# Optimization experiments

Measured on AMD Instinct MI355X. Metric: run time of the kernel, lower is better.

Reference implementation:

```python
import jax, jax.numpy as jnp
import numpy as np

BSZ, N, D = 32, 243, 544   # batch, frames, embed dim (17 joints * 32)
H = 8                      # heads
HD = D // H                # head dim = 68
NS = 17                    # number of seeds (joints)
UP = 2                     # ExAttention up_ratio
MLP1 = 4 * D               # Block MLP hidden (mlp_ratio=4)
MLP2 = 2 * D               # ExtBaseBlock MLP hidden (mlp_ratio=2)


def _ln(x, g, b):
    m = x.mean(-1, keepdims=True)
    v = ((x - m) ** 2).mean(-1, keepdims=True)
    return (x - m) * jax.lax.rsqrt(v + 1e-5) * g + b


def _lin(x, W, b=None):
    y = x @ W.T
    return y if b is None else y + b


def _mlp(x, w1, b1, w2, b2):
    return _lin(jax.nn.gelu(_lin(x, w1, b1), approximate=False), w2, b2)


def setup_inputs() -> dict:
    key = jax.random.key(0)
    ks = jax.random.split(key, 40)
    i = iter(range(40))
    r = lambda shape, s=0.02: jax.random.normal(ks[next(i)], shape, jnp.float32) * s
    inp = {
        'x': jax.random.normal(ks[next(i)], (BSZ, N, D), jnp.float32),
        'seed': jax.random.normal(ks[next(i)], (NS, D), jnp.float32),
        # --- RelativeAttention block (use_swin=True, qkv_bias=False) ---
        'ln1_g': jnp.ones((D,), jnp.float32), 'ln1_b': jnp.zeros((D,), jnp.float32),
        'w_qkv': r((3 * D, D)),
        'w_proj': r((D, D)), 'b_proj': jnp.zeros((D,), jnp.float32),
        'b_table': r((1, H, 2 * N - 1)),  # trunc_normal std=0.02 table
        'ln2_g': jnp.ones((D,), jnp.float32), 'ln2_b': jnp.zeros((D,), jnp.float32),
        'mlp_w1': r((MLP1, D)), 'mlp_b1': jnp.zeros((MLP1,), jnp.float32),
        'mlp_w2': r((D, MLP1)), 'mlp_b2': jnp.zeros((D,), jnp.float32),
        # --- ExtBaseBlock (ExAttention, up_ratio=2, mlp_ratio=2) ---
        'eln1_g': jnp.ones((D,), jnp.float32), 'eln1_b': jnp.zeros((D,), jnp.float32),
        'w_trans': r((UP * D, D)), 'b_trans': jnp.zeros((UP * D,), jnp.float32),
        'w0': r((UP * D, D)), 'b0': jnp.zeros((UP * D,), jnp.float32),
        'w1': r((UP * D, D)), 'b1': jnp.zeros((UP * D,), jnp.float32),
        'w_proj2': r((D, UP * D)), 'b_proj2': jnp.zeros((D,), jnp.float32),
        'eln2_g': jnp.ones((D,), jnp.float32), 'eln2_b': jnp.zeros((D,), jnp.float32),
        'emlp_w1': r((MLP2, D)), 'emlp_b1': jnp.zeros((MLP2,), jnp.float32),
        'emlp_w2': r((D, MLP2)), 'emlp_b2': jnp.zeros((D,), jnp.float32),
    }
    return inp


def reference(x, seed, ln1_g, ln1_b, w_qkv, w_proj, b_proj, b_table,
              ln2_g, ln2_b, mlp_w1, mlp_b1, mlp_w2, mlp_b2,
              eln1_g, eln1_b, w_trans, b_trans, w0, b0, w1, b1,
              w_proj2, b_proj2, eln2_g, eln2_b, emlp_w1, emlp_b1, emlp_w2, emlp_b2):
    Bsz, Nn, C = x.shape
    # ---------- Block with RelativeAttention (use_swin=True) ----------
    h = _ln(x, ln1_g, ln1_b)
    qkv = _lin(h, w_qkv).reshape(Bsz, Nn, 3, H, HD).transpose(2, 0, 3, 1, 4)
    q, k, v = qkv[0], qkv[1], qkv[2]                        # (B,H,N,hd)
    # Swin-style relative position bias gather: B_index[i,j] = i - j + N - 1
    idx = jnp.arange(Nn)[:, None] - jnp.arange(Nn)[None, :] + (Nn - 1)
    bias = b_table[:, :, idx]                               # (1,H,N,N)
    attn = jax.nn.softmax(jnp.einsum('bhid,bhjd->bhij', q, k) * (HD ** -0.5) + bias, axis=-1)
    o = jnp.einsum('bhij,bhjd->bhid', attn, v).transpose(0, 2, 1, 3).reshape(Bsz, Nn, C)
    x = x + _lin(o, w_proj, b_proj)
    x = x + _mlp(_ln(x, ln2_g, ln2_b), mlp_w1, mlp_b1, mlp_w2, mlp_b2)
    # ---------- ExtBaseBlock with ExAttention (double-softmax external memory) ----------
    h = _ln(x, eln1_g, eln1_b)
    uc = UP * C // H                                         # per-head up dim = 136
    xu = _lin(h, w_trans, b_trans).reshape(Bsz, Nn, H, uc).transpose(0, 2, 1, 3)  # (B,H,F,uc)
    s0 = _lin(seed, w0, b0).reshape(NS, H, uc).transpose(1, 0, 2)                 # (H,NS,uc)
    a = jnp.einsum('bhfc,hnc->bhfn', xu, s0)                 # (B,H,F,NS)
    a = jax.nn.softmax(a, axis=-2)                           # softmax over frame axis
    a = a / (1e-7 + a.sum(-1, keepdims=True))                # renormalize over seeds
    mean_attn = a.mean(axis=(0, 1, 2))                       # (NS,)
    s1 = _lin(seed, w1, b1).reshape(NS, H, uc).transpose(1, 0, 2)                 # (H,NS,uc)
    o = jnp.einsum('bhfn,hnc->bhfc', a, s1).transpose(0, 2, 1, 3).reshape(Bsz, Nn, UP * C)
    x = x + _lin(o, w_proj2, b_proj2)
    x = x + _mlp(_ln(x, eln2_g, eln2_b), emlp_w1, emlp_b1, emlp_w2, emlp_b2)
    return x, mean_attn
```

## Files before the change

### kernel.cpp

```cpp
#include <hip/hip_runtime.h>
#include <math.h>
#include <stdint.h>

#define BSZd 32
#define NTOK 243
#define DIMd 544
#define NH 8
#define HDd 68
#define NSEED 17
#define UPDd 1088
#define UCd 136
#define MROWS (BSZd*NTOK)
#define BND ((size_t)MROWS*DIMd)
#define QPP 24576
#define KPOFF ((size_t)256*QPP)
#define VTP 20480
#define PBP 65536
#define BUFE (128*32)
#define SLICE 6144

typedef __bf16 bfx8 __attribute__((ext_vector_type(8)));
typedef __bf16 bfx4 __attribute__((ext_vector_type(4)));
typedef float  fx4  __attribute__((ext_vector_type(4)));

#define GLOAD_LDS(g, l) __builtin_amdgcn_global_load_lds( \
    (__attribute__((address_space(1))) void*)(g), \
    (__attribute__((address_space(3))) void*)(l), 16, 0, 0)

__device__ __forceinline__ void mfma_core(const __bf16* __restrict__ A, int lda,
        const __bf16* __restrict__ W, int ldb, int K,
        __bf16* __restrict__ As, __bf16* __restrict__ Bs, fx4 acc[4][4]) {
    const int tid = threadIdx.x;
    const int lane = tid & 63, wave = tid >> 6;
    const int r = lane >> 2, cp = lane & 3;
    const int c = cp ^ (r & 3) ^ ((r >> 2) & 1);
    const __bf16* Ag0 = A + (size_t)(wave * 32 + r) * lda + c * 8;
    const __bf16* Ag1 = Ag0 + (size_t)16 * lda;
    const __bf16* Wg0 = W + (size_t)(wave * 32 + r) * ldb + c * 8;
    const __bf16* Wg1 = Wg0 + (size_t)16 * ldb;
    const int wr0 = (wave * 32) * 32;
    const int wr1 = (wave * 32 + 16) * 32;
    const int fl = lane & 15, q = lane >> 4;
    const int wm = (wave & 1) * 64, wn = (wave >> 1) * 64;
    const int sw = (fl & 3) ^ ((fl >> 2) & 1);
    const int IT = K >> 5;
    GLOAD_LDS(Ag0, As + wr0);
    GLOAD_LDS(Ag1, As + wr1);
    GLOAD_LDS(Wg0, Bs + wr0);
    GLOAD_LDS(Wg1, Bs + wr1);
    for (int kit = 0; kit < IT; kit++) {
        const int p = kit & 1;
        __syncthreads();
        if (kit + 1 < IT) {
            const int np = 1 - p;
            const int off = (kit + 1) * 32;
            GLOAD_LDS(Ag0 + off, As + np * BUFE + wr0);
            GLOAD_LDS(Ag1 + off, As + np * BUFE + wr1);
            GLOAD_LDS(Wg0 + off, Bs + np * BUFE + wr0);
            GLOAD_LDS(Wg1 + off, Bs + np * BUFE + wr1);
        }
        const __bf16* Ab = As + p * BUFE;
        const __bf16* Bb = Bs + p * BUFE;
        bfx8 af[4], bfr[4];
        #pragma unroll
        for (int i = 0; i < 4; i++) {
            int m = wm + i * 16 + fl;
            af[i] = *(const bfx8*)(Ab + (m * 4 + (q ^ sw)) * 8);
            int n = wn + i * 16 + fl;
            bfr[i] = *(const bfx8*)(Bb + (n * 4 + (q ^ sw)) * 8);
        }
        #pragma unroll
        for (int i = 0; i < 4; i++)
            #pragma unroll
            for (int j = 0; j < 4; j++)
                acc[i][j] = __builtin_amdgcn_mfma_f32_16x16x32_bf16(af[i], bfr[j], acc[i][j], 0, 0, 0);
    }
}

struct Cvt8 {
    const float* src[8];
    __bf16* dst[8];
    int nreal[8];
    int rows[8];
    int K[8];
};
__global__ __launch_bounds__(256) void cvt_all(Cvt8 d) {
    int blk = blockIdx.x;
    int seg = 0, base = 0;
    while (seg < 7 && blk - base >= d.rows[seg]) { base += d.rows[seg]; seg++; }
    int n = blk - base;
    int K = d.K[seg];
    __bf16* drow = d.dst[seg] + (size_t)n * K;
    if (n < d.nreal[seg]) {
        const float* srow = d.src[seg] + (size_t)n * K;
        for (int k = threadIdx.x * 4; k < K; k += 1024) {
            float4 v = *(const float4*)(srow + k);
            bfx4 o; o[0]=(__bf16)v.x; o[1]=(__bf16)v.y; o[2]=(__bf16)v.z; o[3]=(__bf16)v.w;
            *(bfx4*)(drow + k) = o;
        }
    } else {
        bfx4 z = {(__bf16)0.f,(__bf16)0.f,(__bf16)0.f,(__bf16)0.f};
        for (int k = threadIdx.x * 4; k < K; k += 1024) *(bfx4*)(drow + k) = z;
    }
}

__global__ __launch_bounds__(256) void zero4(float4* __restrict__ p, int n4) {
    float4 z = make_float4(0.f, 0.f, 0.f, 0.f);
    for (int i = blockIdx.x * 256 + threadIdx.x; i < n4; i += gridDim.x * 256)
        p[i] = z;
}

__global__ __launch_bounds__(256) void ln_kernel(const float* __restrict__ x,
        const float* __restrict__ g, const float* __restrict__ bb, __bf16* __restrict__ out) {
    int row = blockIdx.x;
    const float* xr = x + (size_t)row * DIMd;
    __bf16* orow = out + (size_t)row * DIMd;
    int tid = threadIdx.x;
    float e0 = xr[tid];
    float e1 = xr[tid + 256];
    float e2 = (tid < DIMd - 512) ? xr[tid + 512] : 0.f;
    float s  = e0 + e1 + e2;
    float sq = e0*e0 + e1*e1 + e2*e2;
    __shared__ float sa[4], sb[4];
    for (int off = 32; off; off >>= 1) { s += __shfl_down(s, off, 64); sq += __shfl_down(sq, off, 64); }
    int lane = tid & 63, w = tid >> 6;
    if (lane == 0) { sa[w] = s; sb[w] = sq; }
    __syncthreads();
    if (tid == 0) { sa[0] = sa[0]+sa[1]+sa[2]+sa[3]; sb[0] = sb[0]+sb[1]+sb[2]+sb[3]; }
    __syncthreads();
    s = sa[0]; sq = sb[0];
    float mean = s * (1.f / DIMd);
    float var  = sq * (1.f / DIMd) - mean * mean;
    float rstd = rsqrtf(var + 1e-5f);
    orow[tid]       = (__bf16)((e0 - mean) * rstd * g[tid]       + bb[tid]);
    orow[tid + 256] = (__bf16)((e1 - mean) * rstd * g[tid + 256] + bb[tid + 256]);
    if (tid < DIMd - 512)
        orow[tid + 512] = (__bf16)((e2 - mean) * rstd * g[tid + 512] + bb[tid + 512]);
}

template<int ACT, int HAS_BIAS, int HAS_RES, int OUTMODE>
__global__ __launch_bounds__(256) void mgemm(
        const __bf16* __restrict__ A, int lda, const __bf16* __restrict__ W, int ldb,
        const float* __restrict__ bias, const float* __restrict__ res,
        void* __restrict__ Cv, int M, int Mtiles, int Nreal, int K, int Cstride,
        __bf16* __restrict__ qQK, __bf16* __restrict__ qVt) {
    const int L = blockIdx.y * gridDim.x + blockIdx.x;
    const int xcd = L & 7, s = L >> 3;
    const int kk2 = s / gridDim.x, j2 = s - kk2 * gridDim.x;
    const int mt = kk2 * 8 + xcd;
    if (mt >= Mtiles) return;
    const int m0 = mt * 64, n0 = j2 * 128;
    __shared__ __bf16 Smem[2 * SLICE];
    const int tid = threadIdx.x, lane = tid & 63, w = tid >> 6;
    const __bf16* Gs[3];
    int dbase[3];
    #pragma unroll
    for (int it = 0; it < 3; it++) {
        int ch = w * 192 + it * 64 + lane;
        int row = ch >> 2, cp2 = ch & 3;
        int cc = cp2 ^ (row & 3) ^ ((row >> 2) & 1);
        dbase[it] = (w * 192 + it * 64) * 8;
        Gs[it] = (row < 64) ? A + (size_t)(m0 + row) * lda + cc * 8
                            : W + (size_t)(n0 + row - 64) * ldb + cc * 8;
    }
    const int fl = lane & 15, q = lane >> 4;
    const int wm = (w & 1) * 32, wn = (w >> 1) * 64;
    const int sw = (fl & 3) ^ ((fl >> 2) & 1);
    const int IT = K >> 5;
    fx4 acc[2][4];
    #pragma unroll
    for (int i = 0; i < 2; i++)
        #pragma unroll
        for (int j = 0; j < 4; j++)
            acc[i][j] = (fx4){0.f, 0.f, 0.f, 0.f};
    #pragma unroll
    for (int it = 0; it < 3; it++)
        GLOAD_LDS(Gs[it], Smem + dbase[it]);
    for (int kit = 0; kit < IT; kit++) {
        const int p = kit & 1;
        __syncthreads();
        if (kit + 1 < IT) {
            const int np = 1 - p;
            const int koff = (kit + 1) * 32;
            #pragma unroll
            for (int it = 0; it < 3; it++)
                GLOAD_LDS(Gs[it] + koff, Smem + np * SLICE + dbase[it]);
        }
        const __bf16* Ab = Smem + p * SLICE;
        const __bf16* Bb = Ab + 2048;
        bfx8 af[2], bfr[4];
        #pragma unroll
        for (int i = 0; i < 2; i++) {
            int m = wm + i * 16 + fl;
            af[i] = *(const bfx8*)(Ab + (m * 4 + (q ^ sw)) * 8);
        }
        #pragma unroll
        for (int j = 0; j < 4; j++) {
            int n = wn + j * 16 + fl;
            bfr[j] = *(const bfx8*)(Bb + (n * 4 + (q ^ sw)) * 8);
        }
        #pragma unroll
        for (int i = 0; i < 2; i++)
            #pragma unroll
            for (int j = 0; j < 4; j++)
                acc[i][j] = __builtin_amdgcn_mfma_f32_16x16x32_bf16(af[i], bfr[j], acc[i][j], 0, 0, 0);
    }
    #pragma unroll
    for (int i = 0; i < 2; i++)
        #pragma unroll
        for (int v = 0; v < 4; v++) {
            int row = m0 + wm + i * 16 + q * 4 + v;
            if (row >= M) continue;
            #pragma unroll
            for (int j = 0; j < 4; j++) {
                int col = n0 + wn + j * 16 + fl;
                if (col >= Nreal) continue;
                float val = acc[i][j][v];
                if (HAS_BIAS) val += bias[col];
                if (ACT == 1) val = 0.5f * val * (1.f + erff(val * 0.70710678118654752f));
                if (HAS_RES)  val += res[(size_t)row * Cstride + col];
                if (OUTMODE == 2) {
                    int t = col / DIMd, rem = col - t * DIMd;
                    int hh = rem / HDd, hd = rem - hh * HDd;
                    int b = row / NTOK, tok = row - b * NTOK;
                    int bh = b * 8 + hh;
                    if (t == 0)      qQK[(size_t)bh * QPP + tok * 96 + hd] = (__bf16)val;
                    else if (t == 1) qQK[KPOFF + (size_t)bh * QPP + tok * 96 + hd] = (__bf16)val;
                    else             qVt[(size_t)bh * VTP + hd * 256 + tok] = (__bf16)val;
                } else if (OUTMODE == 1) {
                    ((__bf16*)Cv)[(size_t)row * Cstride + col] = (__bf16)val;
                } else {
                    ((float*)Cv)[(size_t)row * Cstride + col] = val;
                }
            }
        }
}

__global__ __launch_bounds__(256) void gemm32_kernel(
        const float* __restrict__ A, const float* __restrict__ W,
        const float* __restrict__ bias, float* __restrict__ C, int M, int Nn, int K) {
    __shared__ __align__(16) float As[16][68];
    __shared__ __align__(16) float Ws[16][68];
    int tid = threadIdx.x;
    int tx = tid & 15, ty = tid >> 4;
    int m0 = blockIdx.y * 64, n0 = blockIdx.x * 64;
    float acc[4][4] = {};
    int lr = tid >> 2, lk = (tid & 3) << 2;
    for (int k0 = 0; k0 < K; k0 += 16) {
        float4 av = make_float4(0.f,0.f,0.f,0.f), wv = make_float4(0.f,0.f,0.f,0.f);
        int gm = m0 + lr, gn = n0 + lr, gk = k0 + lk;
        if (gm < M)  av = *(const float4*)(A + (size_t)gm * K + gk);
        if (gn < Nn) wv = *(const float4*)(W + (size_t)gn * K + gk);
        __syncthreads();
        As[lk+0][lr]=av.x; As[lk+1][lr]=av.y; As[lk+2][lr]=av.z; As[lk+3][lr]=av.w;
        Ws[lk+0][lr]=wv.x; Ws[lk+1][lr]=wv.y; Ws[lk+2][lr]=wv.z; Ws[lk+3][lr]=wv.w;
        __syncthreads();
        #pragma unroll
        for (int kk = 0; kk < 16; kk++) {
            float4 a4 = *(const float4*)&As[kk][ty << 2];
            float4 b4 = *(const float4*)&Ws[kk][tx << 2];
            float ar[4] = {a4.x, a4.y, a4.z, a4.w};
            float br[4] = {b4.x, b4.y, b4.z, b4.w};
            #pragma unroll
            for (int i = 0; i < 4; i++)
                #pragma unroll
                for (int j = 0; j < 4; j++)
                    acc[i][j] = fmaf(ar[i], br[j], acc[i][j]);
        }
    }
    #pragma unroll
    for (int i = 0; i < 4; i++) {
        int gm = m0 + (ty << 2) + i;
        if (gm >= M) continue;
        #pragma unroll
        for (int j = 0; j < 4; j++) {
            int gn = n0 + (tx << 2) + j;
            if (gn >= Nn) continue;
            C[(size_t)gm * Nn + gn] = acc[i][j] + bias[gn];
        }
    }
}

__global__ __launch_bounds__(256) void attn_escore(const __bf16* __restrict__ Qp,
        const float* __restrict__ bt, __bf16* __restrict__ Pb, float* __restrict__ rs) {
    __shared__ __bf16 Qs[128 * 96];
    __shared__ __bf16 Ks[256 * 96];
    __shared__ float sumb[128 * 2];
    const int mh = blockIdx.x, bh = blockIdx.y, h = bh & 7;
    const int tid = threadIdx.x, lane = tid & 63, w = tid >> 6;
    const int fl = lane & 15, q = lane >> 4;
    const int wm = (w & 1) * 64, wn = (w >> 1) * 128;
    const __bf16* Qg = Qp + (size_t)bh * QPP + (size_t)mh * 128 * 96;
    const __bf16* Kg = Qp + KPOFF + (size_t)bh * QPP;
    #pragma unroll
    for (int it = 0; it < 6; it++) {
        int Lc = (w * 6 + it) * 64 + lane;
        int r = Lc / 12, sl = Lc - r * 12, c = sl ^ (r & 3);
        GLOAD_LDS(Qg + r * 96 + c * 8, Qs + Lc * 8);
    }
    #pragma unroll
    for (int it = 0; it < 12; it++) {
        int Lc = (w * 12 + it) * 64 + lane;
        int r = Lc / 12, sl = Lc - r * 12, c = sl ^ (r & 3);
        GLOAD_LDS(Kg + r * 96 + c * 8, Ks + Lc * 8);
    }
    __syncthreads();
    fx4 acc[4][8];
    #pragma unroll
    for (int i = 0; i < 4; i++)
        #pragma unroll
        for (int jj = 0; jj < 8; jj++)
            acc[i][jj] = (fx4){0.f, 0.f, 0.f, 0.f};
    #pragma unroll
    for (int kk = 0; kk < 3; kk++) {
        bfx8 af[4], bfr[8];
        #pragma unroll
        for (int i = 0; i < 4; i++) {
            int rA = wm + i * 16 + fl, cA = kk * 4 + q;
            af[i] = *(const bfx8*)(Qs + (rA * 12 + (cA ^ (rA & 3))) * 8);
        }
        #pragma unroll
        for (int jj = 0; jj < 8; jj++) {
            int rB = wn + jj * 16 + fl, cB = kk * 4 + q;
            bfr[jj] = *(const bfx8*)(Ks + (rB * 12 + (cB ^ (rB & 3))) * 8);
        }
        #pragma unroll
        for (int i = 0; i < 4; i++)
            #pragma unroll
            for (int jj = 0; jj < 8; jj++)
                acc[i][jj] = __builtin_amdgcn_mfma_f32_16x16x32_bf16(af[i], bfr[jj], acc[i][jj], 0, 0, 0);
    }
    const float scale = 0.121267812518166f;
    const float* btr = bt + h * (2 * NTOK - 1);
    __bf16* Pp = Pb + (size_t)bh * PBP + (size_t)mh * 128 * 256;
    #pragma unroll
    for (int i = 0; i < 4; i++)
        #pragma unroll
        for (int v = 0; v < 4; v++) {
            int lr = wm + i * 16 + q * 4 + v;
            int gm = mh * 128 + lr;
            float sm = 0.f;
            #pragma unroll
            for (int jj = 0; jj < 8; jj++) {
                int gn = wn + jj * 16 + fl;
                float e = 0.f;
                if (gm < NTOK && gn < NTOK)
                    e = expf(acc[i][jj][v] * scale + btr[gm - gn + NTOK - 1]);
                acc[i][jj][v] = e;
                sm += e;
                Pp[(size_t)lr * 256 + gn] = (__bf16)e;
            }
            #pragma unroll
            for (int msk = 1; msk < 16; msk <<= 1)
                sm += __shfl_xor(sm, msk, 64);
            if (fl == 0) sumb[lr * 2 + (w >> 1)] = sm;
        }
    __syncthreads();
    if (tid < 128)
        rs[(size_t)bh * 256 + mh * 128 + tid] = sumb[tid * 2] + sumb[tid * 2 + 1];
}

__global__ __launch_bounds__(256) void attn_pv2(const __bf16* __restrict__ Pb,
        const __bf16* __restrict__ Vt, const float* __restrict__ rs,
        __bf16* __restrict__ o) {
    __shared__ __bf16 As[2 * BUFE];
    __shared__ __bf16 Bs[2 * BUFE];
    const int mt = blockIdx.x, bh = blockIdx.y, b = bh >> 3, h = bh & 7;
    const int tid = threadIdx.x, lane = tid & 63, wave = tid >> 6;
    fx4 acc[4][4];
    #pragma unroll
    for (int i = 0; i < 4; i++)
        #pragma unroll
        for (int j = 0; j < 4; j++)
            acc[i][j] = (fx4){0.f, 0.f, 0.f, 0.f};
    mfma_core(Pb + (size_t)bh * PBP + (size_t)mt * 128 * 256, 256,
              Vt + (size_t)bh * VTP, 256, 256, As, Bs, acc);
    const int fl = lane & 15, q = lane >> 4;
    const int wm = (wave & 1) * 64, wn = (wave >> 1) * 64;
    #pragma unroll
    for (int i = 0; i < 4; i++)
        #pragma unroll
        for (int v = 0; v < 4; v++) {
            int gm = mt * 128 + wm + i * 16 + q * 4 + v;
            if (gm >= NTOK) continue;
            float inv = 1.f / rs[(size_t)bh * 256 + gm];
            #pragma unroll
            for (int j = 0; j < 4; j++) {
                int col = wn + j * 16 + fl;
                if (col >= HDd) continue;
                o[((size_t)(b * NTOK + gm)) * DIMd + h * HDd + col] = (__bf16)(acc[i][j][v] * inv);
            }
        }
}

__global__ __launch_bounds__(256) void scatter_s0big(const float* __restrict__ S0f,
        __bf16* __restrict__ W) {
    int hn = blockIdx.x;
    __bf16* row = W + (size_t)hn * UPDd;
    int h = hn / NSEED, n = hn - h * NSEED;
    for (int j = threadIdx.x; j < UPDd; j += 256) {
        __bf16 v = (__bf16)0.f;
        if (hn < 136 && (j / UCd) == h) v = (__bf16)S0f[(size_t)n * UPDd + j];
        row[j] = v;
    }
}

__global__ __launch_bounds__(256) void scatter_s1bigT(const float* __restrict__ S1f,
        __bf16* __restrict__ W) {
    int j = blockIdx.x;
    __bf16* row = W + (size_t)j * 160;
    int hj = j / UCd;
    int t = threadIdx.x;
    if (t < 160) {
        __bf16 v = (__bf16)0.f;
        if (j < UPDd && t < 136) {
            int h = t / NSEED, n = t - h * NSEED;
            if (h == hj) v = (__bf16)S1f[(size_t)n * UPDd + j];
        }
        row[t] = v;
    }
}

__global__ __launch_bounds__(256) void seed_softmax2(float* __restrict__ a2) {
    int col = blockIdx.x, b = blockIdx.y;
    float* base = a2 + (size_t)b * NTOK * 136 + col;
    int f = threadIdx.x;
    __shared__ float rbuf[4];
    float v = (f < NTOK) ? base[(size_t)f * 136] : -1e30f;
    float m = v;
    for (int off = 32; off; off >>= 1) m = fmaxf(m, __shfl_down(m, off, 64));
    int lane = f & 63, w = f >> 6;
    if (lane == 0) rbuf[w] = m;
    __syncthreads();
    m = fmaxf(fmaxf(rbuf[0], rbuf[1]), fmaxf(rbuf[2], rbuf[3]));
    float e = (f < NTOK) ? expf(v - m) : 0.f;
    float s = e;
    for (int off = 32; off; off >>= 1) s += __shfl_down(s, off, 64);
    __syncthreads();
    if (lane == 0) rbuf[w] = s;
    __syncthreads();
    float denom = rbuf[0] + rbuf[1] + rbuf[2] + rbuf[3];
    if (f < NTOK) base[(size_t)f * 136] = e / denom;
}

__global__ void zero_kernel(float* p, int n) {
    int i = blockIdx.x * blockDim.x + threadIdx.x;
    if (i < n) p[i] = 0.f;
}

__global__ __launch_bounds__(256) void seed_renorm(const float* __restrict__ a2,
        __bf16* __restrict__ a2b, float* __restrict__ part) {
    int f = blockIdx.x, b = blockIdx.y;
    int t = threadIdx.x;
    __shared__ float vals[136];
    __shared__ float hinv[8];
    __shared__ float nsum[NSEED];
    if (t < NSEED) nsum[t] = 0.f;
    const float* arow = a2 + ((size_t)(b * NTOK + f)) * 136;
    if (t < 136) vals[t] = arow[t];
    __syncthreads();
    if (t < 8) {
        float s = 0.f;
        #pragma unroll
        for (int n = 0; n < NSEED; n++) s += vals[t * NSEED + n];
        hinv[t] = 1.f / (1e-7f + s);
    }
    __syncthreads();
    __bf16* brow = a2b + ((size_t)(b * NTOK + f)) * 160;
    if (t < 160) {
        if (t < 136) {
            float wv = vals[t] * hinv[t / NSEED];
            brow[t] = (__bf16)wv;
            atomicAdd(&nsum[t % NSEED], wv);
        } else brow[t] = (__bf16)0.f;
    }
    __syncthreads();
    if (t < NSEED) atomicAdd(&part[b * NSEED + t], nsum[t]);
}

__global__ void mean_final(const float* __restrict__ part, float* __restrict__ mean_attn) {
    int n = threadIdx.x;
    if (n < NSEED) {
        float s = 0.f;
        for (int b = 0; b < BSZd; b++) s += part[b * NSEED + n];
        mean_attn[n] = s * (1.f / (BSZd * NH * NTOK));
    }
}

extern "C" void kernel_launch(void* const* d_in, const int* in_sizes, int n_in,
                              void* d_out, int out_size, void* d_ws, size_t ws_size,
                              hipStream_t stream) {
    (void)in_sizes; (void)n_in; (void)out_size; (void)ws_size;
    const float* x       = (const float*)d_in[0];
    const float* seed    = (const float*)d_in[1];
    const float* ln1_g   = (const float*)d_in[2];
    const float* ln1_b   = (const float*)d_in[3];
    const float* w_qkv   = (const float*)d_in[4];
    const float* w_proj  = (const float*)d_in[5];
    const float* b_proj  = (const float*)d_in[6];
    const float* b_table = (const float*)d_in[7];
    const float* ln2_g   = (const float*)d_in[8];
    const float* ln2_b   = (const float*)d_in[9];
    const float* mlp_w1  = (const float*)d_in[10];
    const float* mlp_b1  = (const float*)d_in[11];
    const float* mlp_w2  = (const float*)d_in[12];
    const float* mlp_b2  = (const float*)d_in[13];
    const float* eln1_g  = (const float*)d_in[14];
    const float* eln1_b  = (const float*)d_in[15];
    const float* w_trans = (const float*)d_in[16];
    const float* b_trans = (const float*)d_in[17];
    const float* w0      = (const float*)d_in[18];
    const float* b0      = (const float*)d_in[19];
    const float* w1      = (const float*)d_in[20];
    const float* b1      = (const float*)d_in[21];
    const float* w_proj2 = (const float*)d_in[22];
    const float* b_proj2 = (const float*)d_in[23];
    const float* eln2_g  = (const float*)d_in[24];
    const float* eln2_b  = (const float*)d_in[25];
    const float* emlp_w1 = (const float*)d_in[26];
    const float* emlp_b1 = (const float*)d_in[27];
    const float* emlp_w2 = (const float*)d_in[28];
    const float* emlp_b2 = (const float*)d_in[29];

    char* wsb = (char*)d_ws;
    __bf16* Wq  = (__bf16*)(wsb);
    __bf16* Wp  = (__bf16*)(wsb + 1810432);
    __bf16* Wm1 = (__bf16*)(wsb + 2506752);
    __bf16* Wm2 = (__bf16*)(wsb + 4874240);
    __bf16* Wt  = (__bf16*)(wsb + 7659520);
    __bf16* Wp2 = (__bf16*)(wsb + 8912896);
    __bf16* We1 = (__bf16*)(wsb + 10305536);
    __bf16* We2 = (__bf16*)(wsb + 11558912);
    __bf16* Abf = (__bf16*)(wsb + 12951552);
    float*  F1  = (float*) (wsb + 21446656);
    float*  F2  = (float*) (wsb + 38367232);
    char*   RegBig = wsb + 55287808;
    char*   RegS   = wsb + 89266176;
    __bf16* Qp  = (__bf16*)RegBig;
    __bf16* Pb  = (__bf16*)F1;
    __bf16* Vt  = (__bf16*)RegS;
    float*  rsb = (float*)(RegS + 10485760);
    __bf16* Tb   = (__bf16*)RegBig;
    __bf16* XU   = (__bf16*)RegBig;
    __bf16* O2   = (__bf16*)(RegBig + 16920576);
    __bf16* T2   = (__bf16*)RegBig;
    float*  a2    = (float*)RegS;
    __bf16* a2b   = (__bf16*)(RegS + 4230144);
    float*  S0f   = (float*)(RegS + 6728704);
    float*  S1f   = (float*)(RegS + 6802688);
    __bf16* S0big = (__bf16*)(RegS + 6876672);
    __bf16* S1bigT= (__bf16*)(RegS + 7433728);
    float*  mean_part = (float*)(RegS + 7802368);
    float* xout = (float*)d_out;
    float* mean_attn = xout + BND;

    dim3 blk(256);
    Cvt8 cd;
    cd.src[0]=w_qkv;  cd.dst[0]=Wq;  cd.nreal[0]=1632; cd.rows[0]=1664; cd.K[0]=544;
    cd.src[1]=w_proj; cd.dst[1]=Wp;  cd.nreal[1]=544;  cd.rows[1]=640;  cd.K[1]=544;
    cd.src[2]=mlp_w1; cd.dst[2]=Wm1; cd.nreal[2]=2176; cd.rows[2]=2176; cd.K[2]=544;
    cd.src[3]=mlp_w2; cd.dst[3]=Wm2; cd.nreal[3]=544;  cd.rows[3]=640;  cd.K[3]=2176;
    cd.src[4]=w_trans;cd.dst[4]=Wt;  cd.nreal[4]=1088; cd.rows[4]=1152; cd.K[4]=544;
    cd.src[5]=w_proj2;cd.dst[5]=Wp2; cd.nreal[5]=544;  cd.rows[5]=640;  cd.K[5]=1088;
    cd.src[6]=emlp_w1;cd.dst[6]=We1; cd.nreal[6]=1088; cd.rows[6]=1152; cd.K[6]=544;
    cd.src[7]=emlp_w2;cd.dst[7]=We2; cd.nreal[7]=544;  cd.rows[7]=640;  cd.K[7]=1088;
    cvt_all<<<8704, blk, 0, stream>>>(cd);
    zero4<<<1024, blk, 0, stream>>>((float4*)Qp, 1572864);
    zero4<<<1024, blk, 0, stream>>>((float4*)Vt, 655360);
    ln_kernel<<<MROWS, blk, 0, stream>>>(x, ln1_g, ln1_b, Abf);
    mgemm<0,0,0,2><<<dim3(13,128), blk, 0, stream>>>(Abf, 544, Wq, 544, nullptr, nullptr, nullptr, MROWS, 122, 1632, 544, 0, Qp, Vt);
    attn_escore<<<dim3(2,256), blk, 0, stream>>>(Qp, b_table, Pb, rsb);
    attn_pv2<<<dim3(2,256), blk, 0, stream>>>(Pb, Vt, rsb, Abf);
    mgemm<0,1,1,0><<<dim3(5,128), blk, 0, stream>>>(Abf, 544, Wp, 544, b_proj, x, F1, MROWS, 122, 544, 544, 544, nullptr, nullptr);
    ln_kernel<<<MROWS, blk, 0, stream>>>(F1, ln2_g, ln2_b, Abf);
    mgemm<1,1,0,1><<<dim3(17,128), blk, 0, stream>>>(Abf, 544, Wm1, 544, mlp_b1, nullptr, Tb, MROWS, 122, 2176, 544, 2176, nullptr, nullptr);
    mgemm<0,1,1,0><<<dim3(5,128), blk, 0, stream>>>(Tb, 2176, Wm2, 2176, mlp_b2, F1, F2, MROWS, 122, 544, 2176, 544, nullptr, nullptr);
    ln_kernel<<<MROWS, blk, 0, stream>>>(F2, eln1_g, eln1_b, Abf);
    mgemm<0,1,0,1><<<dim3(9,128), blk, 0, stream>>>(Abf, 544, Wt, 544, b_trans, nullptr, XU, MROWS, 122, 1088, 544, 1088, nullptr, nullptr);
    gemm32_kernel<<<dim3(17,1), blk, 0, stream>>>(seed, w0, b0, S0f, NSEED, UPDd, DIMd);
    gemm32_kernel<<<dim3(17,1), blk, 0, stream>>>(seed, w1, b1, S1f, NSEED, UPDd, DIMd);
    scatter_s0big<<<256, blk, 0, stream>>>(S0f, S0big);
    scatter_s1bigT<<<1152, blk, 0, stream>>>(S1f, S1bigT);
    mgemm<0,0,0,0><<<dim3(2,128), blk, 0, stream>>>(XU, 1088, S0big, 1088, nullptr, nullptr, a2, MROWS, 122, 136, 1088, 136, nullptr, nullptr);
    seed_softmax2<<<dim3(136,BSZd), blk, 0, stream>>>(a2);
    zero_kernel<<<3, blk, 0, stream>>>(mean_part, BSZd * NSEED);
    seed_renorm<<<dim3(NTOK,BSZd), blk, 0, stream>>>(a2, a2b, mean_part);
    mean_final<<<1, 32, 0, stream>>>(mean_part, mean_attn);
    mgemm<0,0,0,1><<<dim3(9,128), blk, 0, stream>>>(a2b, 160, S1bigT, 160, nullptr, nullptr, O2, MROWS, 122, 1088, 160, 1088, nullptr, nullptr);
    mgemm<0,1,1,0><<<dim3(5,128), blk, 0, stream>>>(O2, 1088, Wp2, 1088, b_proj2, F2, F1, MROWS, 122, 544, 1088, 544, nullptr, nullptr);
    ln_kernel<<<MROWS, blk, 0, stream>>>(F1, eln2_g, eln2_b, Abf);
    mgemm<1,1,0,1><<<dim3(9,128), blk, 0, stream>>>(Abf, 544, We1, 544, emlp_b1, nullptr, T2, MROWS, 122, 1088, 544, 1088, nullptr, nullptr);
    mgemm<0,1,1,0><<<dim3(5,128), blk, 0, stream>>>(T2, 1088, We2, 1088, emlp_b2, F1, xout, MROWS, 122, 544, 1088, 544, nullptr, nullptr);
}
```

Measured before the change: 673.9 us.

## Deepen GEMM LDS pipeline to 4 stages and fuse prep kernels into one launch

The main mgemm kernel moves from a double buffer to a four-slot LDS ring that prefetches two K-steps ahead, using explicit vmcnt waits and raw barriers instead of __syncthreads. The goal is to hide more global-load latency behind MFMA work. Separately, weight conversion, zeroing, the seed projections and the S0/S1 scatter are merged into a single prep kernel, and the seed buffers move to new scratch offsets, which removes several small launches. LDS use per block doubles, which may lower occupancy.

Result: faster. 631.9 us (-6.2%).

```diff
diff --git a/kernel.cpp b/kernel.cpp
--- a/kernel.cpp
+++ b/kernel.cpp
@@ -77,37 +77,112 @@
     }
 }
 
-struct Cvt8 {
-    const float* src[8];
-    __bf16* dst[8];
-    int nreal[8];
-    int rows[8];
-    int K[8];
+struct PrepArgs {
+    const float* csrc[8];
+    __bf16* cdst[8];
+    int cnreal[8];
+    int crows[8];
+    int cK[8];
+    const float* seed;
+    const float* w0; const float* b0;
+    const float* w1; const float* b1;
+    __bf16* S0big; __bf16* S1bigT;
+    float4* zQp; float4* zVt; float4* zS1pad; float4* zMean;
 };
-__global__ __launch_bounds__(256) void cvt_all(Cvt8 d) {
+
+__global__ __launch_bounds__(256) void prep(PrepArgs d) {
     int blk = blockIdx.x;
-    int seg = 0, base = 0;
-    while (seg < 7 && blk - base >= d.rows[seg]) { base += d.rows[seg]; seg++; }
-    int n = blk - base;
-    int K = d.K[seg];
-    __bf16* drow = d.dst[seg] + (size_t)n * K;
-    if (n < d.nreal[seg]) {
-        const float* srow = d.src[seg] + (size_t)n * K;
-        for (int k = threadIdx.x * 4; k < K; k += 1024) {
-            float4 v = *(const float4*)(srow + k);
-            bfx4 o; o[0]=(__bf16)v.x; o[1]=(__bf16)v.y; o[2]=(__bf16)v.z; o[3]=(__bf16)v.w;
-            *(bfx4*)(drow + k) = o;
+    const int tid = threadIdx.x;
+    if (blk < 8704) {
+        int seg = 0, base = 0;
+        while (seg < 7 && blk - base >= d.crows[seg]) { base += d.crows[seg]; seg++; }
+        int n = blk - base;
+        int K = d.cK[seg];
+        __bf16* drow = d.cdst[seg] + (size_t)n * K;
+        if (n < d.cnreal[seg]) {
+            const float* srow = d.csrc[seg] + (size_t)n * K;
+            for (int k = tid * 4; k < K; k += 1024) {
+                float4 v = *(const float4*)(srow + k);
+                bfx4 o; o[0]=(__bf16)v.x; o[1]=(__bf16)v.y; o[2]=(__bf16)v.z; o[3]=(__bf16)v.w;
+                *(bfx4*)(drow + k) = o;
+            }
+        } else {
+            bfx4 z = {(__bf16)0.f,(__bf16)0.f,(__bf16)0.f,(__bf16)0.f};
+            for (int k = tid * 4; k < K; k += 1024) *(bfx4*)(drow + k) = z;
+        }
+        return;
+    }
+    blk -= 8704;
+    if (blk < 1024) {
+        float4 z = make_float4(0.f, 0.f, 0.f, 0.f);
+        for (size_t i = (size_t)blk * 256 + tid; i < 1572864; i += 262144) d.zQp[i] = z;
+        for (size_t i = (size_t)blk * 256 + tid; i < 655360;  i += 262144) d.zVt[i] = z;
+        for (size_t i = (size_t)blk * 256 + tid; i < 1280;    i += 262144) d.zS1pad[i] = z;
+        for (size_t i = (size_t)blk * 256 + tid; i < 136;     i += 262144) d.zMean[i] = z;
+        return;
+    }
+    blk -= 1024;
+    const int variant = blk / 17;
+    const int n0 = (blk - variant * 17) * 64;
+    const float* W    = variant ? d.w1 : d.w0;
+    const float* bias = variant ? d.b1 : d.b0;
+    __shared__ __align__(16) float As[16][68];
+    __shared__ __align__(16) float Ws[16][68];
+    __shared__ float stash[17][68];
+    int tx = tid & 15, ty = tid >> 4;
+    float acc[4][4] = {};
+    int lr = tid >> 2, lk = (tid & 3) << 2;
+    for (int k0 = 0; k0 < 544; k0 += 16) {
+        float4 av = make_float4(0.f,0.f,0.f,0.f);
+        float4 wv;
+        int gk = k0 + lk;
+        if (lr < 17) av = *(const float4*)(d.seed + (size_t)lr * 544 + gk);
+        wv = *(const float4*)(W + (size_t)(n0 + lr) * 544 + gk);
+        __syncthreads();
+        As[lk+0][lr]=av.x; As[lk+1][lr]=av.y; As[lk+2][lr]=av.z; As[lk+3][lr]=av.w;
+        Ws[lk+0][lr]=wv.x; Ws[lk+1][lr]=wv.y; Ws[lk+2][lr]=wv.z; Ws[lk+3][lr]=wv.w;
+        __syncthreads();
+        #pragma unroll
+        for (int kk = 0; kk < 16; kk++) {
+            float4 a4 = *(const float4*)&As[kk][ty << 2];
+            float4 b4 = *(const float4*)&Ws[kk][tx << 2];
+            float ar[4] = {a4.x, a4.y, a4.z, a4.w};
+            float br[4] = {b4.x, b4.y, b4.z, b4.w};
+            #pragma unroll
+            for (int i = 0; i < 4; i++)
+                #pragma unroll
+                for (int j = 0; j < 4; j++)
+                    acc[i][j] = fmaf(ar[i], br[j], acc[i][j]);
+        }
+    }
+    #pragma unroll
+    for (int i = 0; i < 4; i++) {
+        int gm = (ty << 2) + i;
+        if (gm < 17)
+            #pragma unroll
+            for (int j = 0; j < 4; j++)
+                stash[gm][(tx << 2) + j] = acc[i][j] + bias[n0 + (tx << 2) + j];
+    }
+    __syncthreads();
+    if (variant == 0) {
+        for (int idx = tid; idx < 256 * 64; idx += 256) {
+            int hn = idx >> 6, jo = idx & 63;
+            int j = n0 + jo;
+            int h = j / UCd;
+            int dd = hn - h * NSEED;
+            __bf16 v = (dd >= 0 && dd < NSEED) ? (__bf16)stash[dd][jo] : (__bf16)0.f;
+            d.S0big[(size_t)hn * UPDd + j] = v;
         }
     } else {
-        bfx4 z = {(__bf16)0.f,(__bf16)0.f,(__bf16)0.f,(__bf16)0.f};
-        for (int k = threadIdx.x * 4; k < K; k += 1024) *(bfx4*)(drow + k) = z;
-    }
-}
-
-__global__ __launch_bounds__(256) void zero4(float4* __restrict__ p, int n4) {
-    float4 z = make_float4(0.f, 0.f, 0.f, 0.f);
-    for (int i = blockIdx.x * 256 + threadIdx.x; i < n4; i += gridDim.x * 256)
-        p[i] = z;
+        for (int idx = tid; idx < 64 * 160; idx += 256) {
+            int jo = idx / 160, t = idx - jo * 160;
+            int j = n0 + jo;
+            int hj = j / UCd;
+            int dd = t - hj * NSEED;
+            __bf16 v = (dd >= 0 && dd < NSEED) ? (__bf16)stash[dd][jo] : (__bf16)0.f;
+            d.S1bigT[(size_t)j * 160 + t] = v;
+        }
+    }
 }
 
 __global__ __launch_bounds__(256) void ln_kernel(const float* __restrict__ x,
@@ -150,7 +225,7 @@
     const int mt = kk2 * 8 + xcd;
     if (mt >= Mtiles) return;
     const int m0 = mt * 64, n0 = j2 * 128;
-    __shared__ __bf16 Smem[2 * SLICE];
+    __shared__ __bf16 Smem[4 * SLICE];
     const int tid = threadIdx.x, lane = tid & 63, w = tid >> 6;
     const __bf16* Gs[3];
     int dbase[3];
@@ -173,20 +248,8 @@
         #pragma unroll
         for (int j = 0; j < 4; j++)
             acc[i][j] = (fx4){0.f, 0.f, 0.f, 0.f};
-    #pragma unroll
-    for (int it = 0; it < 3; it++)
-        GLOAD_LDS(Gs[it], Smem + dbase[it]);
-    for (int kit = 0; kit < IT; kit++) {
-        const int p = kit & 1;
-        __syncthreads();
-        if (kit + 1 < IT) {
-            const int np = 1 - p;
-            const int koff = (kit + 1) * 32;
-            #pragma unroll
-            for (int it = 0; it < 3; it++)
-                GLOAD_LDS(Gs[it] + koff, Smem + np * SLICE + dbase[it]);
-        }
-        const __bf16* Ab = Smem + p * SLICE;
+    auto compute = [&](int pidx) {
+        const __bf16* Ab = Smem + pidx * SLICE;
         const __bf16* Bb = Ab + 2048;
         bfx8 af[2], bfr[4];
         #pragma unroll
@@ -204,7 +267,34 @@
             #pragma unroll
             for (int j = 0; j < 4; j++)
                 acc[i][j] = __builtin_amdgcn_mfma_f32_16x16x32_bf16(af[i], bfr[j], acc[i][j], 0, 0, 0);
-    }
+    };
+    #pragma unroll
+    for (int sl = 0; sl < 2; sl++)
+        #pragma unroll
+        for (int it = 0; it < 3; it++)
+            GLOAD_LDS(Gs[it] + sl * 32, Smem + sl * SLICE + dbase[it]);
+    int kit = 0;
+    for (; kit < IT - 2; kit++) {
+        {
+            const int koff = (kit + 2) * 32;
+            __bf16* dst = Smem + ((kit + 2) & 3) * SLICE;
+            #pragma unroll
+            for (int it = 0; it < 3; it++)
+                GLOAD_LDS(Gs[it] + koff, dst + dbase[it]);
+        }
+        asm volatile("s_waitcnt vmcnt(6)" ::: "memory");
+        __builtin_amdgcn_s_barrier();
+        __builtin_amdgcn_sched_barrier(0);
+        compute(kit & 3);
+    }
+    asm volatile("s_waitcnt vmcnt(3)" ::: "memory");
+    __builtin_amdgcn_s_barrier();
+    __builtin_amdgcn_sched_barrier(0);
+    compute((IT - 2) & 3);
+    asm volatile("s_waitcnt vmcnt(0)" ::: "memory");
+    __builtin_amdgcn_s_barrier();
+    __builtin_amdgcn_sched_barrier(0);
+    compute((IT - 1) & 3);
     #pragma unroll
     for (int i = 0; i < 2; i++)
         #pragma unroll
@@ -236,51 +326,6 @@
         }
 }
 
-__global__ __launch_bounds__(256) void gemm32_kernel(
-        const float* __restrict__ A, const float* __restrict__ W,
-        const float* __restrict__ bias, float* __restrict__ C, int M, int Nn, int K) {
-    __shared__ __align__(16) float As[16][68];
-    __shared__ __align__(16) float Ws[16][68];
-    int tid = threadIdx.x;
-    int tx = tid & 15, ty = tid >> 4;
-    int m0 = blockIdx.y * 64, n0 = blockIdx.x * 64;
-    float acc[4][4] = {};
-    int lr = tid >> 2, lk = (tid & 3) << 2;
-    for (int k0 = 0; k0 < K; k0 += 16) {
-        float4 av = make_float4(0.f,0.f,0.f,0.f), wv = make_float4(0.f,0.f,0.f,0.f);
-        int gm = m0 + lr, gn = n0 + lr, gk = k0 + lk;
-        if (gm < M)  av = *(const float4*)(A + (size_t)gm * K + gk);
-        if (gn < Nn) wv = *(const float4*)(W + (size_t)gn * K + gk);
-        __syncthreads();
-        As[lk+0][lr]=av.x; As[lk+1][lr]=av.y; As[lk+2][lr]=av.z; As[lk+3][lr]=av.w;
-        Ws[lk+0][lr]=wv.x; Ws[lk+1][lr]=wv.y; Ws[lk+2][lr]=wv.z; Ws[lk+3][lr]=wv.w;
-        __syncthreads();
-        #pragma unroll
-        for (int kk = 0; kk < 16; kk++) {
-            float4 a4 = *(const float4*)&As[kk][ty << 2];
-            float4 b4 = *(const float4*)&Ws[kk][tx << 2];
-            float ar[4] = {a4.x, a4.y, a4.z, a4.w};
-            float br[4] = {b4.x, b4.y, b4.z, b4.w};
-            #pragma unroll
-            for (int i = 0; i < 4; i++)
-                #pragma unroll
-                for (int j = 0; j < 4; j++)
-                    acc[i][j] = fmaf(ar[i], br[j], acc[i][j]);
-        }
-    }
-    #pragma unroll
-    for (int i = 0; i < 4; i++) {
-        int gm = m0 + (ty << 2) + i;
-        if (gm >= M) continue;
-        #pragma unroll
-        for (int j = 0; j < 4; j++) {
-            int gn = n0 + (tx << 2) + j;
-            if (gn >= Nn) continue;
-            C[(size_t)gm * Nn + gn] = acc[i][j] + bias[gn];
-        }
-    }
-}
-
 __global__ __launch_bounds__(256) void attn_escore(const __bf16* __restrict__ Qp,
         const float* __restrict__ bt, __bf16* __restrict__ Pb, float* __restrict__ rs) {
     __shared__ __bf16 Qs[128 * 96];
@@ -393,34 +438,6 @@
         }
 }
 
-__global__ __launch_bounds__(256) void scatter_s0big(const float* __restrict__ S0f,
-        __bf16* __restrict__ W) {
-    int hn = blockIdx.x;
-    __bf16* row = W + (size_t)hn * UPDd;
-    int h = hn / NSEED, n = hn - h * NSEED;
-    for (int j = threadIdx.x; j < UPDd; j += 256) {
-        __bf16 v = (__bf16)0.f;
-        if (hn < 136 && (j / UCd) == h) v = (__bf16)S0f[(size_t)n * UPDd + j];
-        row[j] = v;
-    }
-}
-
-__global__ __launch_bounds__(256) void scatter_s1bigT(const float* __restrict__ S1f,
-        __bf16* __restrict__ W) {
-    int j = blockIdx.x;
-    __bf16* row = W + (size_t)j * 160;
-    int hj = j / UCd;
-    int t = threadIdx.x;
-    if (t < 160) {
-        __bf16 v = (__bf16)0.f;
-        if (j < UPDd && t < 136) {
-            int h = t / NSEED, n = t - h * NSEED;
-            if (h == hj) v = (__bf16)S1f[(size_t)n * UPDd + j];
-        }
-        row[t] = v;
-    }
-}
-
 __global__ __launch_bounds__(256) void seed_softmax2(float* __restrict__ a2) {
     int col = blockIdx.x, b = blockIdx.y;
     float* base = a2 + (size_t)b * NTOK * 136 + col;
@@ -441,11 +458,6 @@
     __syncthreads();
     float denom = rbuf[0] + rbuf[1] + rbuf[2] + rbuf[3];
     if (f < NTOK) base[(size_t)f * 136] = e / denom;
-}
-
-__global__ void zero_kernel(float* p, int n) {
-    int i = blockIdx.x * blockDim.x + threadIdx.x;
-    if (i < n) p[i] = 0.f;
 }
 
 __global__ __launch_bounds__(256) void seed_renorm(const float* __restrict__ a2,
@@ -540,33 +552,34 @@
     __bf16* Pb  = (__bf16*)F1;
     __bf16* Vt  = (__bf16*)RegS;
     float*  rsb = (float*)(RegS + 10485760);
+    __bf16* S0big = (__bf16*)(RegS + 10747904);
+    __bf16* S1bigT= (__bf16*)(RegS + 11304960);
+    float*  mean_part = (float*)(RegS + 11673600);
     __bf16* Tb   = (__bf16*)RegBig;
     __bf16* XU   = (__bf16*)RegBig;
     __bf16* O2   = (__bf16*)(RegBig + 16920576);
     __bf16* T2   = (__bf16*)RegBig;
     float*  a2    = (float*)RegS;
     __bf16* a2b   = (__bf16*)(RegS + 4230144);
-    float*  S0f   = (float*)(RegS + 6728704);
-    float*  S1f   = (float*)(RegS + 6802688);
-    __bf16* S0big = (__bf16*)(RegS + 6876672);
-    __bf16* S1bigT= (__bf16*)(RegS + 7433728);
-    float*  mean_part = (float*)(RegS + 7802368);
     float* xout = (float*)d_out;
     float* mean_attn = xout + BND;
 
     dim3 blk(256);
-    Cvt8 cd;
-    cd.src[0]=w_qkv;  cd.dst[0]=Wq;  cd.nreal[0]=1632; cd.rows[0]=1664; cd.K[0]=544;
-    cd.src[1]=w_proj; cd.dst[1]=Wp;  cd.nreal[1]=544;  cd.rows[1]=640;  cd.K[1]=544;
-    cd.src[2]=mlp_w1; cd.dst[2]=Wm1; cd.nreal[2]=2176; cd.rows[2]=2176; cd.K[2]=544;
-    cd.src[3]=mlp_w2; cd.dst[3]=Wm2; cd.nreal[3]=544;  cd.rows[3]=640;  cd.K[3]=2176;
-    cd.src[4]=w_trans;cd.dst[4]=Wt;  cd.nreal[4]=1088; cd.rows[4]=1152; cd.K[4]=544;
-    cd.src[5]=w_proj2;cd.dst[5]=Wp2; cd.nreal[5]=544;  cd.rows[5]=640;  cd.K[5]=1088;
-    cd.src[6]=emlp_w1;cd.dst[6]=We1; cd.nreal[6]=1088; cd.rows[6]=1152; cd.K[6]=544;
-    cd.src[7]=emlp_w2;cd.dst[7]=We2; cd.nreal[7]=544;  cd.rows[7]=640;  cd.K[7]=1088;
-    cvt_all<<<8704, blk, 0, stream>>>(cd);
-    zero4<<<1024, blk, 0, stream>>>((float4*)Qp, 1572864);
-    zero4<<<1024, blk, 0, stream>>>((float4*)Vt, 655360);
+    PrepArgs pa;
+    pa.csrc[0]=w_qkv;  pa.cdst[0]=Wq;  pa.cnreal[0]=1632; pa.crows[0]=1664; pa.cK[0]=544;
+    pa.csrc[1]=w_proj; pa.cdst[1]=Wp;  pa.cnreal[1]=544;  pa.crows[1]=640;  pa.cK[1]=544;
+    pa.csrc[2]=mlp_w1; pa.cdst[2]=Wm1; pa.cnreal[2]=2176; pa.crows[2]=2176; pa.cK[2]=544;
+    pa.csrc[3]=mlp_w2; pa.cdst[3]=Wm2; pa.cnreal[3]=544;  pa.crows[3]=640;  pa.cK[3]=2176;
+    pa.csrc[4]=w_trans;pa.cdst[4]=Wt;  pa.cnreal[4]=1088; pa.crows[4]=1152; pa.cK[4]=544;
+    pa.csrc[5]=w_proj2;pa.cdst[5]=Wp2; pa.cnreal[5]=544;  pa.crows[5]=640;  pa.cK[5]=1088;
+    pa.csrc[6]=emlp_w1;pa.cdst[6]=We1; pa.cnreal[6]=1088; pa.crows[6]=1152; pa.cK[6]=544;
+    pa.csrc[7]=emlp_w2;pa.cdst[7]=We2; pa.cnreal[7]=544;  pa.crows[7]=640;  pa.cK[7]=1088;
+    pa.seed = seed; pa.w0 = w0; pa.b0 = b0; pa.w1 = w1; pa.b1 = b1;
+    pa.S0big = S0big; pa.S1bigT = S1bigT;
+    pa.zQp = (float4*)Qp; pa.zVt = (float4*)Vt;
+    pa.zS1pad = (float4*)(S1bigT + (size_t)1088 * 160);
+    pa.zMean = (float4*)mean_part;
+    prep<<<9762, blk, 0, stream>>>(pa);
     ln_kernel<<<MROWS, blk, 0, stream>>>(x, ln1_g, ln1_b, Abf);
     mgemm<0,0,0,2><<<dim3(13,128), blk, 0, stream>>>(Abf, 544, Wq, 544, nullptr, nullptr, nullptr, MROWS, 122, 1632, 544, 0, Qp, Vt);
     attn_escore<<<dim3(2,256), blk, 0, stream>>>(Qp, b_table, Pb, rsb);
@@ -577,13 +590,8 @@
     mgemm<0,1,1,0><<<dim3(5,128), blk, 0, stream>>>(Tb, 2176, Wm2, 2176, mlp_b2, F1, F2, MROWS, 122, 544, 2176, 544, nullptr, nullptr);
     ln_kernel<<<MROWS, blk, 0, stream>>>(F2, eln1_g, eln1_b, Abf);
     mgemm<0,1,0,1><<<dim3(9,128), blk, 0, stream>>>(Abf, 544, Wt, 544, b_trans, nullptr, XU, MROWS, 122, 1088, 544, 1088, nullptr, nullptr);
-    gemm32_kernel<<<dim3(17,1), blk, 0, stream>>>(seed, w0, b0, S0f, NSEED, UPDd, DIMd);
-    gemm32_kernel<<<dim3(17,1), blk, 0, stream>>>(seed, w1, b1, S1f, NSEED, UPDd, DIMd);
-    scatter_s0big<<<256, blk, 0, stream>>>(S0f, S0big);
-    scatter_s1bigT<<<1152, blk, 0, stream>>>(S1f, S1bigT);
     mgemm<0,0,0,0><<<dim3(2,128), blk, 0, stream>>>(XU, 1088, S0big, 1088, nullptr, nullptr, a2, MROWS, 122, 136, 1088, 136, nullptr, nullptr);
     seed_softmax2<<<dim3(136,BSZd), blk, 0, stream>>>(a2);
-    zero_kernel<<<3, blk, 0, stream>>>(mean_part, BSZd * NSEED);
     seed_renorm<<<dim3(NTOK,BSZd), blk, 0, stream>>>(a2, a2b, mean_part);
     mean_final<<<1, 32, 0, stream>>>(mean_part, mean_attn);
     mgemm<0,0,0,1><<<dim3(9,128), blk, 0, stream>>>(a2b, 160, S1bigT, 160, nullptr, nullptr, O2, MROWS, 122, 1088, 160, 1088, nullptr, nullptr);
```
